# Performance work log

Measured on AMD Instinct MI355X. Metric: run time of the kernel, lower is better.

## Reference

```python
import jax, jax.numpy as jnp
import numpy as np

B, NU, NT = 128, 32, 64          # batch, users/sample, antennas/sample
IN_F, H, OUT_F, NL = 128, 128, 16, 2
N_U, N_A = B * NU, B * NT        # total user / antenna nodes


def setup_inputs() -> dict:
    key = jax.random.key(0)
    ks = iter(jax.random.split(key, 40))
    p = lambda shape: jax.random.normal(next(ks), shape, jnp.float32) * 0.05
    inp = {
        'user_feat': jax.random.normal(next(ks), (N_U, IN_F), jnp.float32),
        'ant_noise': jax.random.normal(next(ks), (N_A, H), jnp.float32),
    }
    # complete bipartite edges within each batch sample
    b = np.arange(B)[:, None, None]
    u = np.arange(NU)[None, :, None]
    t = np.arange(NT)[None, None, :]
    su = np.broadcast_to(b * NU + u, (B, NU, NT)).reshape(-1)  # user global ids
    dt = np.broadcast_to(b * NT + t, (B, NU, NT)).reshape(-1)  # antenna global ids
    inp['src_u2a'] = jnp.asarray(su, jnp.int32)
    inp['dst_u2a'] = jnp.asarray(dt, jnp.int32)
    inp['src_a2u'] = jnp.asarray(dt, jnp.int32)
    inp['dst_a2u'] = jnp.asarray(su, jnp.int32)
    inp['W_ue'] = p((IN_F, H)); inp['b_ue'] = p((H,))
    inp['W_t'] = p((H, H));     inp['b_t'] = p((H,))
    for name in ['ca_aggr', 'ca_self', 'ca_comb', 'cu_aggr', 'cu_self', 'cu_comb']:
        inp[name + '_W'] = p((NL, H, H))
        inp[name + '_b'] = p((NL, H))
    inp['W_norm'] = p((H, OUT_F)); inp['b_norm'] = p((OUT_F,))
    return inp


def mlp(x, W, b):
    # stack of NL Linear(H,H) + ReLU, as in MLP module
    for i in range(W.shape[0]):
        x = jax.nn.relu(x @ W[i] + b[i])
    return x


def rel_conv(src_f, dst_f, src_idx, dst_idx, n_dst, aW, ab, sW, sb, cW, cb):
    # GraphConv2: mean-aggregate mlp_aggr(src) over in-edges, combine with mlp_self(dst)
    msg = mlp(src_f, aW, ab)                                   # [n_src, H]
    summed = jax.ops.segment_sum(msg[src_idx], dst_idx, num_segments=n_dst)
    deg = jax.ops.segment_sum(jnp.ones(dst_idx.shape, jnp.float32), dst_idx,
                              num_segments=n_dst)
    mean = summed / jnp.maximum(deg, 1.0)[:, None]
    return mlp(mlp(dst_f, sW, sb) + mean, cW, cb)


def reference(user_feat, ant_noise, src_u2a, dst_u2a, src_a2u, dst_a2u,
              W_ue, b_ue, W_t, b_t,
              ca_aggr_W, ca_aggr_b, ca_self_W, ca_self_b, ca_comb_W, ca_comb_b,
              cu_aggr_W, cu_aggr_b, cu_self_W, cu_self_b, cu_comb_W, cu_comb_b,
              W_norm, b_norm):
    # InitLayer
    hu = jax.nn.relu(user_feat @ W_ue + b_ue)                  # [B*NU, H]
    ant = jax.nn.relu(hu.reshape(B, NU, H).mean(axis=1) @ W_t + b_t)  # [B, H]
    ha = jnp.repeat(ant, NT, axis=0) + ant_noise               # [B*NT, H]
    # two applications of the SAME HeteroGraphConv (shared weights)
    for _ in range(2):
        na = rel_conv(hu, ha, src_u2a, dst_u2a, N_A,
                      ca_aggr_W, ca_aggr_b, ca_self_W, ca_self_b, ca_comb_W, ca_comb_b)
        nu = rel_conv(ha, hu, src_a2u, dst_a2u, N_U,
                      cu_aggr_W, cu_aggr_b, cu_self_W, cu_self_b, cu_comb_W, cu_comb_b)
        hu, ha = nu, na
    # NormLayer: project, split real/imag, normalize to unit modulus
    y = (ha @ W_norm + b_norm).reshape(B, NT, OUT_F)
    rf = OUT_F // 2
    re, im = y[..., :rf], y[..., rf:]
    mag = jnp.sqrt(re * re + im * im)
    return jnp.concatenate([re / mag, im / mag], axis=-1)      # [B, NT, OUT_F]
```

## Files before the change

kernel.cpp:

```cpp
#include <hip/hip_runtime.h>
#include <math.h>


using frag  = __attribute__((ext_vector_type(8))) short;
using f32x4 = __attribute__((ext_vector_type(4))) float;

#define LDST 136
#define SCOPE_AGT __HIP_MEMORY_SCOPE_AGENT

__device__ __forceinline__ float  bf2f(ushort u) { return __uint_as_float(((unsigned)u) << 16); }
__device__ __forceinline__ ushort f2bf(float f) {
    unsigned u = __float_as_uint(f);
    u += 0x7fff + ((u >> 16) & 1);
    return (ushort)(u >> 16);
}
__device__ __forceinline__ void gst4_sc(void* p, unsigned v) {
    asm volatile("global_store_dword %0, %1, off sc1" :: "v"(p), "v"(v) : "memory");
}

struct GP {
    const float *uf, *noise, *b_ue, *W_t, *b_t;
    const float *Wm[13];
    const float *bias6[6];
    const float *Wn, *bn;
    float *out;
    float *pE, *pA0, *pU0, *pA1;
    unsigned *flg;
};

__device__ __forceinline__ void psync(unsigned* myf, unsigned* pf, unsigned s) {
    asm volatile("s_waitcnt vmcnt(0)" ::: "memory");
    __syncthreads();
    if (threadIdx.x == 0) {
        __hip_atomic_store(myf, s, __ATOMIC_RELAXED, SCOPE_AGT);
        while (__hip_atomic_load(pf, __ATOMIC_RELAXED, SCOPE_AGT) < s)
            __builtin_amdgcn_s_sleep(1);
    }
    __syncthreads();
}

struct PF { float v[32]; };
struct AF { frag f[4]; };
__device__ __forceinline__ PF prefA(const float* __restrict__ W, int n0, int l15, int q) {
    PF p;
    const float* base = W + (size_t)(q * 8) * 128 + n0 + l15;
#pragma unroll
    for (int kc = 0; kc < 4; ++kc)
#pragma unroll
        for (int j = 0; j < 8; ++j)
            p.v[kc * 8 + j] = base[(kc * 32 + j) * 128];
    return p;
}
__device__ __forceinline__ AF convA(const PF& p) {
    AF a;
#pragma unroll
    for (int kc = 0; kc < 4; ++kc) {
        frag f;
#pragma unroll
        for (int j = 0; j < 8; ++j) f[j] = (short)f2bf(p.v[kc * 8 + j]);
        a.f[kc] = f;
    }
    return a;
}

template<int MT, bool MEANADD>
__device__ __forceinline__ void mlp_stage(const AF& A, const ushort* Xl, ushort* Yl,
    const float* biasL, const float* meanL, int n0, int l15, int q)
{
    const float4 bv = *(const float4*)(biasL + n0 + q * 4);
    float4 mv = {0.f, 0.f, 0.f, 0.f};
    if (MEANADD) mv = *(const float4*)(meanL + n0 + q * 4);
#pragma unroll
    for (int mt = 0; mt < MT; ++mt) {
        frag Bv[4];
#pragma unroll
        for (int kc = 0; kc < 4; ++kc)
            Bv[kc] = *(const frag*)(Xl + (mt * 16 + l15) * LDST + kc * 32 + q * 8);
        f32x4 acc = {0.f, 0.f, 0.f, 0.f};
#pragma unroll
        for (int kc = 0; kc < 4; ++kc)
            acc = __builtin_amdgcn_mfma_f32_16x16x32_bf16(A.f[kc], Bv[kc], acc, 0, 0, 0);
        float v0 = acc[0] + bv.x, v1 = acc[1] + bv.y, v2 = acc[2] + bv.z, v3 = acc[3] + bv.w;
        v0 = v0 > 0.f ? v0 : 0.f; v1 = v1 > 0.f ? v1 : 0.f;
        v2 = v2 > 0.f ? v2 : 0.f; v3 = v3 > 0.f ? v3 : 0.f;
        if (MEANADD) { v0 += mv.x; v1 += mv.y; v2 += mv.z; v3 += mv.w; }
        ushort4 o = { f2bf(v0), f2bf(v1), f2bf(v2), f2bf(v3) };
        *(ushort4*)(Yl + (mt * 16 + l15) * LDST + n0 + q * 4) = o;
    }
}

template<int ROWS>
__device__ __forceinline__ void colsum(const ushort* buf, float* redL,
                                       float* ownDst, float* __restrict__ gDst)
{
    const int t = threadIdx.x, g = t >> 7, col = t & 127;
    float s = 0.f;
#pragma unroll
    for (int r = g; r < ROWS; r += 4) s += bf2f(buf[r * LDST + col]);
    redL[g * 128 + col] = s;
    __syncthreads();
    if (t < 128) {
        float tot = redL[t] + redL[128 + t] + redL[256 + t] + redL[384 + t];
        ownDst[t] = tot;
        gst4_sc(gDst + t, __float_as_uint(tot));
    }
    __syncthreads();
}

__global__ __launch_bounds__(512, 1) void k_gnn(GP P)
{
    __shared__ __align__(16) ushort HU[16 * LDST];
    __shared__ __align__(16) ushort HA[32 * LDST];
    __shared__ __align__(16) ushort T0[32 * LDST];
    __shared__ __align__(16) ushort T1[32 * LDST];
    __shared__ __align__(16) float  biasL[1792];
    __shared__ __align__(16) float  redL[512];
    __shared__ __align__(16) float  meanP[128], meanQ[128], antL[128];

    const int blk = blockIdx.x, tid = threadIdx.x;
    const int b = blk >> 1, half = blk & 1, prt = blk ^ 1;
    const int lane = tid & 63, wave = tid >> 6;
    const int q = lane >> 4, l15 = lane & 15;
    const int n0 = wave * 16;
    unsigned* myf = P.flg + blk * 32;
    unsigned* prf = P.flg + prt * 32;

    PF p = prefA(P.Wm[12], n0, l15, q);

    {
        const int r = tid >> 5, k4 = tid & 31;
        const float4 v = *(const float4*)(P.uf + (size_t)(b * 32 + half * 16 + r) * 128 + k4 * 4);
        ushort4 o = { f2bf(v.x), f2bf(v.y), f2bf(v.z), f2bf(v.w) };
        *(ushort4*)(T0 + r * LDST + k4 * 4) = o;
    }
#pragma unroll
    for (int c = tid; c < 1024; c += 512) {
        const int r = c >> 5, k4 = c & 31;
        const float4 v = *(const float4*)(P.noise + (size_t)(b * 64 + half * 32 + r) * 128 + k4 * 4);
        ushort4 o = { f2bf(v.x), f2bf(v.y), f2bf(v.z), f2bf(v.w) };
        *(ushort4*)(HA + r * LDST + k4 * 4) = o;
    }
    if (tid < 128) biasL[tid] = P.b_ue[tid];
    if (tid < 128) biasL[1664 + tid] = P.b_t[tid];
#pragma unroll
    for (int r = 0; r < 6; ++r)
        if (tid < 256) biasL[128 + r * 256 + tid] = P.bias6[r][tid];
    __syncthreads();

    AF A;
    A = convA(p); p = prefA(P.Wm[0], n0, l15, q);
    mlp_stage<1, false>(A, T0, HU, biasL + 0, nullptr, n0, l15, q);
    __syncthreads();
    colsum<16>(HU, redL, meanP, P.pE + blk * 128);
    A = convA(p); p = prefA(P.Wm[1], n0, l15, q);
    mlp_stage<1, false>(A, HU, T0, biasL + 128, nullptr, n0, l15, q);
    __syncthreads();
    A = convA(p); p = prefA(P.Wm[6], n0, l15, q);
    mlp_stage<1, false>(A, T0, T1, biasL + 256, nullptr, n0, l15, q);
    __syncthreads();
    colsum<16>(T1, redL, meanQ, P.pA0 + blk * 128);
    psync(myf, prf, 1u);

    if (tid < 128) {
        meanP[tid] = (meanP[tid] + P.pE[prt * 128 + tid]) * (1.f / 32.f);
        meanQ[tid] = (meanQ[tid] + P.pA0[prt * 128 + tid]) * (1.f / 32.f);
    }
    __syncthreads();
    {
        const int g = tid >> 7, col = tid & 127;
        float s = 0.f;
#pragma unroll 4
        for (int k = g * 32; k < g * 32 + 32; ++k) s += meanP[k] * P.W_t[k * 128 + col];
        redL[g * 128 + col] = s;
    }
    __syncthreads();
    if (tid < 128) {
        float a = biasL[1664 + tid] + redL[tid] + redL[128 + tid] + redL[256 + tid] + redL[384 + tid];
        antL[tid] = a > 0.f ? a : 0.f;
    }
    __syncthreads();
#pragma unroll
    for (int c = tid; c < 1024; c += 512) {
        const int r = c >> 5, k4 = c & 31;
        ushort4 h = *(ushort4*)(HA + r * LDST + k4 * 4);
        ushort4 o = { f2bf(bf2f(h.x) + antL[k4 * 4 + 0]), f2bf(bf2f(h.y) + antL[k4 * 4 + 1]),
                      f2bf(bf2f(h.z) + antL[k4 * 4 + 2]), f2bf(bf2f(h.w) + antL[k4 * 4 + 3]) };
        *(ushort4*)(HA + r * LDST + k4 * 4) = o;
    }
    __syncthreads();

    A = convA(p); p = prefA(P.Wm[7], n0, l15, q);
    mlp_stage<2, false>(A, HA, T0, biasL + 896, nullptr, n0, l15, q);
    __syncthreads();
    A = convA(p); p = prefA(P.Wm[2], n0, l15, q);
    mlp_stage<2, false>(A, T0, T1, biasL + 1024, nullptr, n0, l15, q);
    __syncthreads();
    colsum<32>(T1, redL, meanP, P.pU0 + blk * 128);
    A = convA(p); p = prefA(P.Wm[3], n0, l15, q);
    mlp_stage<2, false>(A, HA, T0, biasL + 384, nullptr, n0, l15, q);
    __syncthreads();
    psync(myf, prf, 2u);
    if (tid < 128)
        meanP[tid] = (meanP[tid] + P.pU0[prt * 128 + tid]) * (1.f / 64.f);
    __syncthreads();
    A = convA(p); p = prefA(P.Wm[4], n0, l15, q);
    mlp_stage<2, true >(A, T0, T1, biasL + 512, meanQ, n0, l15, q);
    __syncthreads();
    A = convA(p); p = prefA(P.Wm[5], n0, l15, q);
    mlp_stage<2, false>(A, T1, T0, biasL + 640, nullptr, n0, l15, q);
    __syncthreads();
    A = convA(p); p = prefA(P.Wm[8], n0, l15, q);
    mlp_stage<2, false>(A, T0, HA, biasL + 768, nullptr, n0, l15, q);
    __syncthreads();
    A = convA(p); p = prefA(P.Wm[9], n0, l15, q);
    mlp_stage<1, false>(A, HU, T0, biasL + 1152, nullptr, n0, l15, q);
    __syncthreads();
    A = convA(p); p = prefA(P.Wm[10], n0, l15, q);
    mlp_stage<1, true >(A, T0, T1, biasL + 1280, meanP, n0, l15, q);
    __syncthreads();
    A = convA(p); p = prefA(P.Wm[11], n0, l15, q);
    mlp_stage<1, false>(A, T1, T0, biasL + 1408, nullptr, n0, l15, q);
    __syncthreads();
    A = convA(p); p = prefA(P.Wm[0], n0, l15, q);
    mlp_stage<1, false>(A, T0, HU, biasL + 1536, nullptr, n0, l15, q);
    __syncthreads();

    A = convA(p); p = prefA(P.Wm[1], n0, l15, q);
    mlp_stage<1, false>(A, HU, T0, biasL + 128, nullptr, n0, l15, q);
    __syncthreads();
    A = convA(p); p = prefA(P.Wm[2], n0, l15, q);
    mlp_stage<1, false>(A, T0, T1, biasL + 256, nullptr, n0, l15, q);
    __syncthreads();
    colsum<16>(T1, redL, meanQ, P.pA1 + blk * 128);
    A = convA(p); p = prefA(P.Wm[3], n0, l15, q);
    mlp_stage<2, false>(A, HA, T0, biasL + 384, nullptr, n0, l15, q);
    __syncthreads();
    psync(myf, prf, 3u);
    if (tid < 128)
        meanQ[tid] = (meanQ[tid] + P.pA1[prt * 128 + tid]) * (1.f / 32.f);
    __syncthreads();
    A = convA(p); p = prefA(P.Wm[4], n0, l15, q);
    mlp_stage<2, true >(A, T0, T1, biasL + 512, meanQ, n0, l15, q);
    __syncthreads();
    A = convA(p); p = prefA(P.Wm[5], n0, l15, q);
    mlp_stage<2, false>(A, T1, T0, biasL + 640, nullptr, n0, l15, q);
    __syncthreads();
    A = convA(p);
    mlp_stage<2, false>(A, T0, T1, biasL + 768, nullptr, n0, l15, q);
    __syncthreads();

    float* WnS = (float*)T0;
    *(float4*)(WnS + tid * 4) = *(const float4*)(P.Wn + tid * 4);
    __syncthreads();
    {
        const int row = tid >> 4, j = tid & 15;
        float acc = P.bn[j];
        const ushort* h = T1 + row * LDST;
#pragma unroll 8
        for (int k = 0; k < 128; ++k) acc += bf2f(h[k]) * WnS[k * 16 + j];
        const float other = __shfl_xor(acc, 8);
        const float mag = sqrtf(acc * acc + other * other);
        P.out[(size_t)(b * 64 + half * 32 + row) * 16 + j] = acc / mag;
    }
}

extern "C" void kernel_launch(void* const* d_in, const int* in_sizes, int n_in,
                              void* d_out, int out_size, void* d_ws, size_t ws_size,
                              hipStream_t stream)
{
    GP P;
    P.uf    = (const float*)d_in[0];
    P.noise = (const float*)d_in[1];
    const float* W_ue = (const float*)d_in[6];
    P.b_ue  = (const float*)d_in[7];
    P.W_t   = (const float*)d_in[8];
    P.b_t   = (const float*)d_in[9];
    const float* caW[3] = {(const float*)d_in[10], (const float*)d_in[12], (const float*)d_in[14]};
    const float* cab[3] = {(const float*)d_in[11], (const float*)d_in[13], (const float*)d_in[15]};
    const float* cuW[3] = {(const float*)d_in[16], (const float*)d_in[18], (const float*)d_in[20]};
    const float* cub[3] = {(const float*)d_in[17], (const float*)d_in[19], (const float*)d_in[21]};
    P.Wn  = (const float*)d_in[22];
    P.bn  = (const float*)d_in[23];
    P.out = (float*)d_out;

    P.Wm[0]  = caW[0]; P.Wm[1]  = caW[0] + 16384;
    P.Wm[2]  = caW[1]; P.Wm[3]  = caW[1] + 16384;
    P.Wm[4]  = caW[2]; P.Wm[5]  = caW[2] + 16384;
    P.Wm[6]  = cuW[0]; P.Wm[7]  = cuW[0] + 16384;
    P.Wm[8]  = cuW[1]; P.Wm[9]  = cuW[1] + 16384;
    P.Wm[10] = cuW[2]; P.Wm[11] = cuW[2] + 16384;
    P.Wm[12] = W_ue;
    P.bias6[0] = cab[0]; P.bias6[1] = cab[1]; P.bias6[2] = cab[2];
    P.bias6[3] = cub[0]; P.bias6[4] = cub[1]; P.bias6[5] = cub[2];

    char* w = (char*)d_ws;
    P.flg = (unsigned*)w;
    P.pE  = (float*)(w + 32768);
    P.pA0 = P.pE  + 256 * 128;
    P.pU0 = P.pA0 + 256 * 128;
    P.pA1 = P.pU0 + 256 * 128;

    hipMemsetAsync(w, 0, 32768, stream);
    k_gnn<<<dim3(256), dim3(512), 0, stream>>>(P);
}
```

Baseline: 132.3 us.

## Reschedule independent MLP stages into paired barrier-free phases with dual weight prefetch

Reorders the chain of MLP stages so that pairs of independent stages (user-side and antenna-side work) run back-to-back between barriers, using separate scratch buffers for the user and antenna paths. Two weight-prefetch registers are kept in flight instead of one, and __syncthreads is replaced by a lighter lgkmcnt-only wait plus s_barrier. The intent is to cut the number of block-wide barriers and hide the latency of weight loads. In exchange it uses more shared memory and registers, and the custom barrier does not wait on outstanding global memory operations.

```diff
diff --git a/kernel.cpp b/kernel.cpp
--- a/kernel.cpp
+++ b/kernel.cpp
@@ -16,6 +16,9 @@
 }
 __device__ __forceinline__ void gst4_sc(void* p, unsigned v) {
     asm volatile("global_store_dword %0, %1, off sc1" :: "v"(p), "v"(v) : "memory");
+}
+__device__ __forceinline__ void bar() {
+    asm volatile("s_waitcnt lgkmcnt(0)\n\ts_barrier" ::: "memory");
 }
 
 struct GP {
@@ -98,21 +101,25 @@
 #pragma unroll
     for (int r = g; r < ROWS; r += 4) s += bf2f(buf[r * LDST + col]);
     redL[g * 128 + col] = s;
-    __syncthreads();
+    bar();
     if (t < 128) {
         float tot = redL[t] + redL[128 + t] + redL[256 + t] + redL[384 + t];
         ownDst[t] = tot;
         gst4_sc(gDst + t, __float_as_uint(tot));
     }
-    __syncthreads();
+    bar();
 }
 
 __global__ __launch_bounds__(512, 1) void k_gnn(GP P)
 {
-    __shared__ __align__(16) ushort HU[16 * LDST];
-    __shared__ __align__(16) ushort HA[32 * LDST];
-    __shared__ __align__(16) ushort T0[32 * LDST];
-    __shared__ __align__(16) ushort T1[32 * LDST];
+    __shared__ __align__(16) ushort HU [16 * LDST];
+    __shared__ __align__(16) ushort HA [32 * LDST];
+    __shared__ __align__(16) ushort TA0[32 * LDST];
+    __shared__ __align__(16) ushort TA1[32 * LDST];
+    __shared__ __align__(16) ushort TA2[32 * LDST];
+    __shared__ __align__(16) ushort TU0[16 * LDST];
+    __shared__ __align__(16) ushort TU1[16 * LDST];
+    __shared__ __align__(16) ushort TU2[16 * LDST];
     __shared__ __align__(16) float  biasL[1792];
     __shared__ __align__(16) float  redL[512];
     __shared__ __align__(16) float  meanP[128], meanQ[128], antL[128];
@@ -125,13 +132,14 @@
     unsigned* myf = P.flg + blk * 32;
     unsigned* prf = P.flg + prt * 32;
 
-    PF p = prefA(P.Wm[12], n0, l15, q);
+    PF pA = prefA(P.Wm[12], n0, l15, q);
+    PF pB = prefA(P.Wm[0],  n0, l15, q);
 
     {
         const int r = tid >> 5, k4 = tid & 31;
         const float4 v = *(const float4*)(P.uf + (size_t)(b * 32 + half * 16 + r) * 128 + k4 * 4);
         ushort4 o = { f2bf(v.x), f2bf(v.y), f2bf(v.z), f2bf(v.w) };
-        *(ushort4*)(T0 + r * LDST + k4 * 4) = o;
+        *(ushort4*)(TA0 + r * LDST + k4 * 4) = o;
     }
 #pragma unroll
     for (int c = tid; c < 1024; c += 512) {
@@ -148,24 +156,25 @@
     __syncthreads();
 
     AF A;
-    A = convA(p); p = prefA(P.Wm[0], n0, l15, q);
-    mlp_stage<1, false>(A, T0, HU, biasL + 0, nullptr, n0, l15, q);
-    __syncthreads();
+    A = convA(pA); pA = prefA(P.Wm[1], n0, l15, q);
+    mlp_stage<1, false>(A, TA0, HU, biasL + 0, nullptr, n0, l15, q);
+    bar();
     colsum<16>(HU, redL, meanP, P.pE + blk * 128);
-    A = convA(p); p = prefA(P.Wm[1], n0, l15, q);
-    mlp_stage<1, false>(A, HU, T0, biasL + 128, nullptr, n0, l15, q);
-    __syncthreads();
-    A = convA(p); p = prefA(P.Wm[6], n0, l15, q);
-    mlp_stage<1, false>(A, T0, T1, biasL + 256, nullptr, n0, l15, q);
-    __syncthreads();
-    colsum<16>(T1, redL, meanQ, P.pA0 + blk * 128);
+    A = convA(pB); pB = prefA(P.Wm[8], n0, l15, q);
+    mlp_stage<1, false>(A, HU, TU0, biasL + 128, nullptr, n0, l15, q);
+    bar();
+    A = convA(pA); pA = prefA(P.Wm[6], n0, l15, q);
+    mlp_stage<1, false>(A, TU0, TU1, biasL + 256, nullptr, n0, l15, q);
+    A = convA(pB); pB = prefA(P.Wm[2], n0, l15, q);
+    mlp_stage<1, false>(A, HU, TU2, biasL + 1152, nullptr, n0, l15, q);
+    bar();
+    colsum<16>(TU1, redL, meanQ, P.pA0 + blk * 128);
     psync(myf, prf, 1u);
-
     if (tid < 128) {
-        meanP[tid] = (meanP[tid] + P.pE[prt * 128 + tid]) * (1.f / 32.f);
+        meanP[tid] = (meanP[tid] + P.pE [prt * 128 + tid]) * (1.f / 32.f);
         meanQ[tid] = (meanQ[tid] + P.pA0[prt * 128 + tid]) * (1.f / 32.f);
     }
-    __syncthreads();
+    bar();
     {
         const int g = tid >> 7, col = tid & 127;
         float s = 0.f;
@@ -173,12 +182,12 @@
         for (int k = g * 32; k < g * 32 + 32; ++k) s += meanP[k] * P.W_t[k * 128 + col];
         redL[g * 128 + col] = s;
     }
-    __syncthreads();
+    bar();
     if (tid < 128) {
         float a = biasL[1664 + tid] + redL[tid] + redL[128 + tid] + redL[256 + tid] + redL[384 + tid];
         antL[tid] = a > 0.f ? a : 0.f;
     }
-    __syncthreads();
+    bar();
 #pragma unroll
     for (int c = tid; c < 1024; c += 512) {
         const int r = c >> 5, k4 = c & 31;
@@ -187,75 +196,65 @@
                       f2bf(bf2f(h.z) + antL[k4 * 4 + 2]), f2bf(bf2f(h.w) + antL[k4 * 4 + 3]) };
         *(ushort4*)(HA + r * LDST + k4 * 4) = o;
     }
-    __syncthreads();
-
-    A = convA(p); p = prefA(P.Wm[7], n0, l15, q);
-    mlp_stage<2, false>(A, HA, T0, biasL + 896, nullptr, n0, l15, q);
-    __syncthreads();
-    A = convA(p); p = prefA(P.Wm[2], n0, l15, q);
-    mlp_stage<2, false>(A, T0, T1, biasL + 1024, nullptr, n0, l15, q);
-    __syncthreads();
-    colsum<32>(T1, redL, meanP, P.pU0 + blk * 128);
-    A = convA(p); p = prefA(P.Wm[3], n0, l15, q);
-    mlp_stage<2, false>(A, HA, T0, biasL + 384, nullptr, n0, l15, q);
-    __syncthreads();
+    bar();
+    A = convA(pA); pA = prefA(P.Wm[7], n0, l15, q);
+    mlp_stage<2, false>(A, HA, TA0, biasL + 896, nullptr, n0, l15, q);
+    A = convA(pB); pB = prefA(P.Wm[3], n0, l15, q);
+    mlp_stage<2, false>(A, HA, TA1, biasL + 384, nullptr, n0, l15, q);
+    bar();
+    A = convA(pA); pA = prefA(P.Wm[4], n0, l15, q);
+    mlp_stage<2, false>(A, TA0, TA2, biasL + 1024, nullptr, n0, l15, q);
+    A = convA(pB); pB = prefA(P.Wm[9], n0, l15, q);
+    mlp_stage<2, true >(A, TA1, HA, biasL + 512, meanQ, n0, l15, q);
+    bar();
+    colsum<32>(TA2, redL, meanP, P.pU0 + blk * 128);
     psync(myf, prf, 2u);
     if (tid < 128)
         meanP[tid] = (meanP[tid] + P.pU0[prt * 128 + tid]) * (1.f / 64.f);
-    __syncthreads();
-    A = convA(p); p = prefA(P.Wm[4], n0, l15, q);
-    mlp_stage<2, true >(A, T0, T1, biasL + 512, meanQ, n0, l15, q);
-    __syncthreads();
-    A = convA(p); p = prefA(P.Wm[5], n0, l15, q);
-    mlp_stage<2, false>(A, T1, T0, biasL + 640, nullptr, n0, l15, q);
-    __syncthreads();
-    A = convA(p); p = prefA(P.Wm[8], n0, l15, q);
-    mlp_stage<2, false>(A, T0, HA, biasL + 768, nullptr, n0, l15, q);
-    __syncthreads();
-    A = convA(p); p = prefA(P.Wm[9], n0, l15, q);
-    mlp_stage<1, false>(A, HU, T0, biasL + 1152, nullptr, n0, l15, q);
-    __syncthreads();
-    A = convA(p); p = prefA(P.Wm[10], n0, l15, q);
-    mlp_stage<1, true >(A, T0, T1, biasL + 1280, meanP, n0, l15, q);
-    __syncthreads();
-    A = convA(p); p = prefA(P.Wm[11], n0, l15, q);
-    mlp_stage<1, false>(A, T1, T0, biasL + 1408, nullptr, n0, l15, q);
-    __syncthreads();
-    A = convA(p); p = prefA(P.Wm[0], n0, l15, q);
-    mlp_stage<1, false>(A, T0, HU, biasL + 1536, nullptr, n0, l15, q);
-    __syncthreads();
-
-    A = convA(p); p = prefA(P.Wm[1], n0, l15, q);
-    mlp_stage<1, false>(A, HU, T0, biasL + 128, nullptr, n0, l15, q);
-    __syncthreads();
-    A = convA(p); p = prefA(P.Wm[2], n0, l15, q);
-    mlp_stage<1, false>(A, T0, T1, biasL + 256, nullptr, n0, l15, q);
-    __syncthreads();
-    colsum<16>(T1, redL, meanQ, P.pA1 + blk * 128);
-    A = convA(p); p = prefA(P.Wm[3], n0, l15, q);
-    mlp_stage<2, false>(A, HA, T0, biasL + 384, nullptr, n0, l15, q);
-    __syncthreads();
+    bar();
+    A = convA(pA); pA = prefA(P.Wm[5], n0, l15, q);
+    mlp_stage<2, false>(A, HA, TA0, biasL + 640, nullptr, n0, l15, q);
+    A = convA(pB); pB = prefA(P.Wm[10], n0, l15, q);
+    mlp_stage<1, true >(A, TU2, TU0, biasL + 1280, meanP, n0, l15, q);
+    bar();
+    A = convA(pA); pA = prefA(P.Wm[11], n0, l15, q);
+    mlp_stage<2, false>(A, TA0, TA1, biasL + 768, nullptr, n0, l15, q);
+    A = convA(pB); pB = prefA(P.Wm[2], n0, l15, q);
+    mlp_stage<1, false>(A, TU0, TU2, biasL + 1408, nullptr, n0, l15, q);
+    bar();
+    A = convA(pA); pA = prefA(P.Wm[0], n0, l15, q);
+    mlp_stage<1, false>(A, TU2, TU0, biasL + 1536, nullptr, n0, l15, q);
+    A = convA(pB); pB = prefA(P.Wm[1], n0, l15, q);
+    mlp_stage<2, false>(A, TA1, TA2, biasL + 384, nullptr, n0, l15, q);
+    bar();
+    A = convA(pA); pA = prefA(P.Wm[3], n0, l15, q);
+    mlp_stage<1, false>(A, TU0, TU1, biasL + 128, nullptr, n0, l15, q);
+    bar();
+    A = convA(pB); pB = prefA(P.Wm[4], n0, l15, q);
+    mlp_stage<1, false>(A, TU1, TU2, biasL + 256, nullptr, n0, l15, q);
+    bar();
+    colsum<16>(TU2, redL, meanQ, P.pA1 + blk * 128);
     psync(myf, prf, 3u);
     if (tid < 128)
         meanQ[tid] = (meanQ[tid] + P.pA1[prt * 128 + tid]) * (1.f / 32.f);
-    __syncthreads();
-    A = convA(p); p = prefA(P.Wm[4], n0, l15, q);
-    mlp_stage<2, true >(A, T0, T1, biasL + 512, meanQ, n0, l15, q);
-    __syncthreads();
-    A = convA(p); p = prefA(P.Wm[5], n0, l15, q);
-    mlp_stage<2, false>(A, T1, T0, biasL + 640, nullptr, n0, l15, q);
-    __syncthreads();
-    A = convA(p);
-    mlp_stage<2, false>(A, T0, T1, biasL + 768, nullptr, n0, l15, q);
-    __syncthreads();
-
-    float* WnS = (float*)T0;
+    bar();
+    A = convA(pA); pA = prefA(P.Wm[5], n0, l15, q);
+    mlp_stage<2, true >(A, TA2, TA0, biasL + 512, meanQ, n0, l15, q);
+    bar();
+    A = convA(pB);
+    mlp_stage<2, false>(A, TA0, TA1, biasL + 640, nullptr, n0, l15, q);
+    bar();
+    A = convA(pA);
+    mlp_stage<2, false>(A, TA1, TA2, biasL + 768, nullptr, n0, l15, q);
+    bar();
+
+    float* WnS = (float*)TA0;
     *(float4*)(WnS + tid * 4) = *(const float4*)(P.Wn + tid * 4);
     __syncthreads();
     {
         const int row = tid >> 4, j = tid & 15;
         float acc = P.bn[j];
-        const ushort* h = T1 + row * LDST;
+        const ushort* h = TA2 + row * LDST;
 #pragma unroll 8
         for (int k = 0; k < 128; ++k) acc += bf2f(h[k]) * WnS[k * 16 + j];
         const float other = __shfl_xor(acc, 8);
```

Measured after the change: 160.0 us. 20.9% more time.
